# Performance work log

Measured on AMD Instinct MI355X. Metric: run time of the kernel, lower is better.

The kernel has to match this reference:

```python
import jax, jax.numpy as jnp
import numpy as np

NUM_HEADS = 12

def setup_inputs() -> dict:
    key = jax.random.key(0)
    k1, k2, k3 = jax.random.split(key, 3)
    B, T, C = 1, 4096, 768
    x = jax.random.normal(k1, (B, T, C), dtype=jnp.float32)
    w_qkv = jax.random.normal(k2, (3 * C, C), dtype=jnp.float32) * (1.0 / np.sqrt(C))
    w_proj = jax.random.normal(k3, (C, C), dtype=jnp.float32) * (1.0 / np.sqrt(C))
    attn_mask = jnp.tril(jnp.ones((T, T), dtype=bool))  # causal block mask
    return {"x": x, "w_qkv": w_qkv, "w_proj": w_proj, "attn_mask": attn_mask}


def reference(x, w_qkv, w_proj, attn_mask):
    B, T, C = x.shape
    H = NUM_HEADS
    Dh = C // H
    # fused QKV projection (torch Linear: y = x @ W.T), then split
    qkv = jnp.einsum('btc,fc->btf', x, w_qkv)  # [B,T,3C]
    q, k, v = jnp.split(qkv, 3, axis=-1)
    # [B,T,C] -> [B,H,T,Dh]
    q = q.reshape(B, T, H, Dh).transpose(0, 2, 1, 3)
    k = k.reshape(B, T, H, Dh).transpose(0, 2, 1, 3)
    v = v.reshape(B, T, H, Dh).transpose(0, 2, 1, 3)
    # masked SDPA, default flex_attention scale = 1/sqrt(head_dim)
    scores = jnp.einsum('bhqd,bhkd->bhqk', q, k) * (1.0 / np.sqrt(Dh))
    neg = jnp.finfo(scores.dtype).min
    scores = jnp.where(attn_mask[None, None, :, :], scores, neg)
    attn = jax.nn.softmax(scores, axis=-1)
    y = jnp.einsum('bhqk,bhkd->bhqd', attn, v)
    # [B,H,T,Dh] -> [B,T,C], then output projection (dropout=0)
    y = y.transpose(0, 2, 1, 3).reshape(B, T, C)
    y = jnp.einsum('btc,fc->btf', y, w_proj)
    return y
```

## Files before the change

### kernel.cpp

```cpp
#include <hip/hip_runtime.h>

typedef unsigned short u16;
typedef unsigned int u32;
typedef __attribute__((ext_vector_type(8))) short s16x8;
typedef __attribute__((ext_vector_type(4))) float f32x4;
typedef __attribute__((ext_vector_type(4))) u16 u16x4;
typedef __attribute__((ext_vector_type(4))) u32 u32x4;

#define LOG2E 1.4426950408889634f

#if __has_builtin(__builtin_amdgcn_exp2f)
#define EXP2F __builtin_amdgcn_exp2f
#else
#define EXP2F exp2f
#endif

__device__ __forceinline__ u16 f32_to_bf16(float f) {
  union { float f; u32 u; } c; c.f = f;
  return (u16)((c.u + 0x7fffu + ((c.u >> 16) & 1u)) >> 16);
}

__device__ __forceinline__ u32 pack_bf16(float lo, float hi) {
  return (u32)f32_to_bf16(lo) | ((u32)f32_to_bf16(hi) << 16);
}

__device__ __forceinline__ void async16(const void* g, void* l) {
  __builtin_amdgcn_global_load_lds(
      (__attribute__((address_space(1))) void*)g,
      (__attribute__((address_space(3))) void*)l, 16, 0, 0);
}

__global__ __launch_bounds__(256) void cast3_f32_bf16(const float* __restrict__ a,
                                                      const float* __restrict__ b,
                                                      const float* __restrict__ c,
                                                      u16* __restrict__ out,
                                                      int n1, int n2, int n3) {
  int i = (blockIdx.x * 256 + threadIdx.x) * 4;
  const float* src;
  int off = i;
  if (i < n1) {
    src = a;
  } else if (i < n1 + n2) {
    src = b; off = i - n1;
  } else if (i < n1 + n2 + n3) {
    src = c; off = i - n1 - n2;
  } else {
    return;
  }
  f32x4 v = *(const f32x4*)(src + off);
  u16x4 o;
  o[0] = f32_to_bf16(v[0]);
  o[1] = f32_to_bf16(v[1]);
  o[2] = f32_to_bf16(v[2]);
  o[3] = f32_to_bf16(v[3]);
  *(u16x4*)(out + i) = o;
}

__device__ __forceinline__ int vt_perm_inv(int k) {
  return (k & 35) | ((k & 16) >> 2) | ((k & 12) << 1);
}

__global__ __launch_bounds__(256) void qkv_gemm(const u16* __restrict__ A,
                                                const u16* __restrict__ B,
                                                u16* __restrict__ qk,
                                                u16* __restrict__ vt) {
  constexpr int K = 768;
  constexpr int BK = 32;
  constexpr int NT = K / BK;
  __shared__ alignas(16) u16 As[2][128 * BK];
  __shared__ alignas(16) u16 Bs[2][128 * BK];
  const int tid = threadIdx.x;
  const int lane = tid & 63;
  const int wid = tid >> 6;
  const int brow = blockIdx.x * 128;
  const int bcol = blockIdx.y * 128;
  const int wr = wid >> 1, wc = wid & 1;
  const int l15 = lane & 15, l4 = lane >> 4;
  f32x4 acc[4][4] = {};
  const int c0 = tid, c1 = tid + 256;
  const int r0 = c0 >> 2, s0 = c0 & 3;
  const int r1 = c1 >> 2, s1 = c1 & 3;

#define G1_STAGE(kt, b)                                                        \
  {                                                                            \
    async16(A + (size_t)(brow + r0) * K + (kt) * BK + s0 * 8, &As[b][c0 * 8]); \
    async16(A + (size_t)(brow + r1) * K + (kt) * BK + s1 * 8, &As[b][c1 * 8]); \
    async16(B + (size_t)(bcol + r0) * K + (kt) * BK + s0 * 8, &Bs[b][c0 * 8]); \
    async16(B + (size_t)(bcol + r1) * K + (kt) * BK + s1 * 8, &Bs[b][c1 * 8]); \
  }

  G1_STAGE(0, 0);
  __syncthreads();
  int cur = 0;
  for (int kt = 0; kt < NT; ++kt) {
    if (kt + 1 < NT) G1_STAGE(kt + 1, cur ^ 1);
    s16x8 af[4], bf[4];
#pragma unroll
    for (int m = 0; m < 4; ++m)
      af[m] = *(const s16x8*)&As[cur][(wr * 64 + m * 16 + l15) * BK + l4 * 8];
#pragma unroll
    for (int n = 0; n < 4; ++n)
      bf[n] = *(const s16x8*)&Bs[cur][(wc * 64 + n * 16 + l15) * BK + l4 * 8];
#pragma unroll
    for (int m = 0; m < 4; ++m)
#pragma unroll
      for (int n = 0; n < 4; ++n)
        acc[m][n] = __builtin_amdgcn_mfma_f32_16x16x32_bf16(af[m], bf[n], acc[m][n], 0, 0, 0);
    __syncthreads();
    cur ^= 1;
  }
#undef G1_STAGE

  const int row0 = brow + wr * 64 + l4 * 4;
  const int col0 = bcol + wc * 64 + l15;
  if (bcol >= 1536) {
#pragma unroll
    for (int m = 0; m < 4; ++m) {
      int t0 = row0 + m * 16;
      int s = (t0 & ~63) + vt_perm_inv(t0 & 63);
#pragma unroll
      for (int n = 0; n < 4; ++n) {
        int vcol = col0 + n * 16 - 1536;
        u16x4 pk;
#pragma unroll
        for (int r = 0; r < 4; ++r) pk[r] = f32_to_bf16(acc[m][n][r]);
        *(u16x4*)&vt[(size_t)vcol * 4096 + s] = pk;
      }
    }
  } else {
#pragma unroll
    for (int m = 0; m < 4; ++m)
#pragma unroll
      for (int n = 0; n < 4; ++n)
#pragma unroll
        for (int r = 0; r < 4; ++r)
          qk[(size_t)(row0 + m * 16 + r) * 1536 + (col0 + n * 16)] =
              f32_to_bf16(acc[m][n][r]);
  }
}

__global__ __launch_bounds__(256) void proj_gemm(const u16* __restrict__ A,
                                                 const u16* __restrict__ B,
                                                 float* __restrict__ C) {
  constexpr int K = 768;
  constexpr int N = 768;
  constexpr int BK = 32;
  constexpr int NT = K / BK;
  __shared__ alignas(16) u16 As[2][128 * BK];
  __shared__ alignas(16) u16 Bs[2][128 * BK];
  const int tid = threadIdx.x;
  const int lane = tid & 63;
  const int wid = tid >> 6;
  const int brow = blockIdx.x * 128;
  const int bcol = blockIdx.y * 128;
  const int wr = wid >> 1, wc = wid & 1;
  const int l15 = lane & 15, l4 = lane >> 4;
  f32x4 acc[4][4] = {};
  const int c0 = tid, c1 = tid + 256;
  const int r0 = c0 >> 2, s0 = c0 & 3;
  const int r1 = c1 >> 2, s1 = c1 & 3;

#define G2_STAGE(kt, b)                                                        \
  {                                                                            \
    async16(A + (size_t)(brow + r0) * K + (kt) * BK + s0 * 8, &As[b][c0 * 8]); \
    async16(A + (size_t)(brow + r1) * K + (kt) * BK + s1 * 8, &As[b][c1 * 8]); \
    async16(B + (size_t)(bcol + r0) * K + (kt) * BK + s0 * 8, &Bs[b][c0 * 8]); \
    async16(B + (size_t)(bcol + r1) * K + (kt) * BK + s1 * 8, &Bs[b][c1 * 8]); \
  }

  G2_STAGE(0, 0);
  __syncthreads();
  int cur = 0;
  for (int kt = 0; kt < NT; ++kt) {
    if (kt + 1 < NT) G2_STAGE(kt + 1, cur ^ 1);
    s16x8 af[4], bf[4];
#pragma unroll
    for (int m = 0; m < 4; ++m)
      af[m] = *(const s16x8*)&As[cur][(wr * 64 + m * 16 + l15) * BK + l4 * 8];
#pragma unroll
    for (int n = 0; n < 4; ++n)
      bf[n] = *(const s16x8*)&Bs[cur][(wc * 64 + n * 16 + l15) * BK + l4 * 8];
#pragma unroll
    for (int m = 0; m < 4; ++m)
#pragma unroll
      for (int n = 0; n < 4; ++n)
        acc[m][n] = __builtin_amdgcn_mfma_f32_16x16x32_bf16(af[m], bf[n], acc[m][n], 0, 0, 0);
    __syncthreads();
    cur ^= 1;
  }
#undef G2_STAGE

  const int row0 = brow + wr * 64 + l4 * 4;
  const int col0 = bcol + wc * 64 + l15;
#pragma unroll
  for (int m = 0; m < 4; ++m)
#pragma unroll
    for (int n = 0; n < 4; ++n)
#pragma unroll
      for (int r = 0; r < 4; ++r)
        C[(size_t)(row0 + m * 16 + r) * N + (col0 + n * 16)] = acc[m][n][r];
}

template <int C>
__global__ __launch_bounds__(256) void attn_kernel(const u16* __restrict__ qk,
                                                   const u16* __restrict__ vt,
                                                   u16* __restrict__ y,
                                                   float* __restrict__ po,
                                                   float* __restrict__ pl) {
  constexpr int MAXCH = 64 / C;
  constexpr int CPH = C * (MAXCH) * (MAXCH + 1) / 2;
  __shared__ alignas(16) u16 Ks[2][64 * 64];
  __shared__ alignas(16) u16 Vs[2][64 * 64];
  const int tid = threadIdx.x;
  const int lane = tid & 63;
  const int wid = tid >> 6;
  const int l15 = lane & 15, l4 = lane >> 4;

  int bx = blockIdx.x;
  int h = bx / CPH;
  int c = CPH - 1 - (bx % CPH);
  int g = 0;
  while (C * (g + 1) * (g + 2) / 2 <= c) ++g;
  int r_ = c - C * g * (g + 1) / 2;
  int qb = g * C + r_ / (g + 1);
  int ch = r_ % (g + 1);
  const int nch = qb / C + 1;

  const int qg = qb * 64 + wid * 16 + l15;
  const float sc = 0.125f * LOG2E;
  const float M_FIX = 16.0f;

  s16x8 bq[2];
#pragma unroll
  for (int ks = 0; ks < 2; ++ks)
    bq[ks] = *(const s16x8*)&qk[(size_t)qg * 1536 + h * 64 + ks * 32 + l4 * 8];

  f32x4 o[4] = {};
  f32x4 lacc = {};

  const u16* Kb = qk + 768 + h * 64;
  const u16* Vb = vt + (size_t)(h * 64) * 4096;

  const int sc0 = tid, sc1 = tid + 256;
  const int sr0 = sc0 >> 3, sp0 = sc0 & 7;
  const int sr1 = sc1 >> 3, sp1 = sc1 & 7;

#define STAGE_KV(t, b)                                                                        \
  {                                                                                           \
    async16(Kb + (size_t)((t) * 64 + sr0) * 1536 + ((sp0 ^ (sr0 & 7)) * 8), &Ks[b][sc0 * 8]); \
    async16(Kb + (size_t)((t) * 64 + sr1) * 1536 + ((sp1 ^ (sr1 & 7)) * 8), &Ks[b][sc1 * 8]); \
    async16(Vb + (size_t)sr0 * 4096 + (t) * 64 + ((sp0 ^ (sr0 & 7)) * 8), &Vs[b][sc0 * 8]);   \
    async16(Vb + (size_t)sr1 * 4096 + (t) * 64 + ((sp1 ^ (sr1 & 7)) * 8), &Vs[b][sc1 * 8]);   \
  }

  const int t0 = ch * C;
  const int t1 = (t0 + C < qb + 1) ? t0 + C : qb + 1;
  STAGE_KV(t0, 0);
  __syncthreads();
  int cur = 0;
  for (int kt = t0; kt < t1; ++kt) {
    if (kt + 1 < t1) STAGE_KV(kt + 1, cur ^ 1);

    f32x4 s4[4];
#pragma unroll
    for (int kf = 0; kf < 4; ++kf) {
      int r = kf * 16 + l15;
      s16x8 k0 = *(const s16x8*)&Ks[cur][r * 64 + ((l4 ^ (r & 7)) * 8)];
      s16x8 k1 = *(const s16x8*)&Ks[cur][r * 64 + (((l4 + 4) ^ (r & 7)) * 8)];
      f32x4 a = {};
      a = __builtin_amdgcn_mfma_f32_16x16x32_bf16(k0, bq[0], a, 0, 0, 0);
      a = __builtin_amdgcn_mfma_f32_16x16x32_bf16(k1, bq[1], a, 0, 0, 0);
      s4[kf] = a;
    }
    if (kt == qb) {
#pragma unroll
      for (int kf = 0; kf < 4; ++kf)
#pragma unroll
        for (int r = 0; r < 4; ++r)
          if (kt * 64 + kf * 16 + l4 * 4 + r > qg) s4[kf][r] = -1e30f;
    }
    u32 w[4][2];
#pragma unroll
    for (int kf = 0; kf < 4; ++kf) {
      f32x4 p;
#pragma unroll
      for (int r = 0; r < 4; ++r)
        p[r] = EXP2F(fmaf(s4[kf][r], sc, -M_FIX));
      lacc += p;
      w[kf][0] = pack_bf16(p[0], p[1]);
      w[kf][1] = pack_bf16(p[2], p[3]);
    }
#pragma unroll
    for (int ks2 = 0; ks2 < 2; ++ks2) {
      u32x4 bu;
      bu[0] = w[2 * ks2][0];
      bu[1] = w[2 * ks2][1];
      bu[2] = w[2 * ks2 + 1][0];
      bu[3] = w[2 * ks2 + 1][1];
      s16x8 bp = __builtin_bit_cast(s16x8, bu);
#pragma unroll
      for (int df = 0; df < 4; ++df) {
        int d = df * 16 + l15;
        int e = ks2 * 4 + l4;
        s16x8 av = *(const s16x8*)&Vs[cur][d * 64 + ((e ^ (d & 7)) * 8)];
        o[df] = __builtin_amdgcn_mfma_f32_16x16x32_bf16(av, bp, o[df], 0, 0, 0);
      }
    }
    __syncthreads();
    cur ^= 1;
  }
#undef STAGE_KV

  float lsum = lacc[0] + lacc[1] + lacc[2] + lacc[3];
  lsum += __shfl_xor(lsum, 16);
  lsum += __shfl_xor(lsum, 32);

  if (nch == 1) {
    float inv = 1.0f / lsum;
#pragma unroll
    for (int df = 0; df < 4; ++df) {
      u16x4 pk;
#pragma unroll
      for (int r = 0; r < 4; ++r) pk[r] = f32_to_bf16(o[df][r] * inv);
      *(u16x4*)&y[(size_t)qg * 768 + h * 64 + df * 16 + l4 * 4] = pk;
    }
  } else {
    const size_t slot = (size_t)(h * 64 + qb) * MAXCH + ch;
    float* ob = po + slot * 4096 + (size_t)(wid * 16 + l15) * 64;
#pragma unroll
    for (int df = 0; df < 4; ++df)
      *(f32x4*)(ob + df * 16 + l4 * 4) = o[df];
    if (lane < 16) pl[slot * 64 + wid * 16 + l15] = lsum;
  }
}

template <int C>
__global__ __launch_bounds__(256) void attn_combine(const float* __restrict__ po,
                                                    const float* __restrict__ pl,
                                                    u16* __restrict__ y) {
  constexpr int MAXCH = 64 / C;
  const int h = blockIdx.x;
  const int qb = C + blockIdx.y;
  const int nch = qb / C + 1;
  const int tid = threadIdx.x;
  const int q = tid >> 2;
  const int d0 = (tid & 3) * 16;

  f32x4 acc[4] = {};
  float lt = 0.f;
  for (int s = 0; s < nch; ++s) {
    const size_t slot = (size_t)(h * 64 + qb) * MAXCH + s;
    lt += pl[slot * 64 + q];
    const float* ob = po + slot * 4096 + (size_t)q * 64 + d0;
#pragma unroll
    for (int j = 0; j < 4; ++j) acc[j] += *(const f32x4*)(ob + j * 4);
  }
  float inv = 1.0f / lt;
  u16* yp = &y[(size_t)(qb * 64 + q) * 768 + h * 64 + d0];
#pragma unroll
  for (int j = 0; j < 4; ++j) {
    u16x4 pk;
#pragma unroll
    for (int r = 0; r < 4; ++r) pk[r] = f32_to_bf16(acc[j][r] * inv);
    *(u16x4*)(yp + j * 4) = pk;
  }
}

extern "C" void kernel_launch(void* const* d_in, const int* in_sizes, int n_in,
                              void* d_out, int out_size, void* d_ws, size_t ws_size,
                              hipStream_t stream) {
  const float* x = (const float*)d_in[0];
  const float* w_qkv = (const float*)d_in[1];
  const float* w_proj = (const float*)d_in[2];
  float* out = (float*)d_out;

  u16* ws = (u16*)d_ws;
  u16* xb = ws;
  u16* wqkvb = xb + 4096 * 768;
  u16* wprojb = wqkvb + 2304 * 768;
  u16* qkb = wprojb + 768 * 768;
  u16* vtb = qkb + (size_t)4096 * 1536;
  u16* yb = vtb + (size_t)768 * 4096;
  const size_t base_u16 = (size_t)4096 * 768 + 2304 * 768 + 768 * 768 +
                          (size_t)4096 * 1536 + (size_t)768 * 4096 + (size_t)4096 * 768;
  float* pf = (float*)(ws + base_u16);
  const size_t base_b = base_u16 * 2;

  constexpr int N1 = 4096 * 768, N2 = 2304 * 768, N3 = 768 * 768;
  cast3_f32_bf16<<<(N1 + N2 + N3) / 4 / 256, 256, 0, stream>>>(
      x, w_qkv, w_proj, xb, N1, N2, N3);

  qkv_gemm<<<dim3(32, 18), 256, 0, stream>>>(xb, wqkvb, qkb, vtb);

  const size_t need16 = base_b + (size_t)(12 * 64 * 4) * (4096 + 64) * 4;
  const size_t need32 = base_b + (size_t)(12 * 64 * 2) * (4096 + 64) * 4;
  if (ws_size >= need16) {
    constexpr int C = 16, MAXCH = 64 / C, CPH = C * MAXCH * (MAXCH + 1) / 2;
    float* po = pf;
    float* pl = po + (size_t)12 * 64 * MAXCH * 4096;
    attn_kernel<C><<<12 * CPH, 256, 0, stream>>>(qkb, vtb, yb, po, pl);
    attn_combine<C><<<dim3(12, 64 - C), 256, 0, stream>>>(po, pl, yb);
  } else if (ws_size >= need32) {
    constexpr int C = 32, MAXCH = 64 / C, CPH = C * MAXCH * (MAXCH + 1) / 2;
    float* po = pf;
    float* pl = po + (size_t)12 * 64 * MAXCH * 4096;
    attn_kernel<C><<<12 * CPH, 256, 0, stream>>>(qkb, vtb, yb, po, pl);
    attn_combine<C><<<dim3(12, 64 - C), 256, 0, stream>>>(po, pl, yb);
  } else {
    constexpr int C = 64, MAXCH = 1, CPH = 64;
    attn_kernel<C><<<12 * CPH, 256, 0, stream>>>(qkb, vtb, yb, nullptr, nullptr);
  }

  proj_gemm<<<dim3(32, 6), 256, 0, stream>>>(yb, wprojb, out);
}
```

Measured before the change: 134.8 us.

## Double query tile per attention block and fold softmax scale into Q projection

```diff
diff --git a/kernel.cpp b/kernel.cpp
--- a/kernel.cpp
+++ b/kernel.cpp
@@ -20,8 +20,10 @@
   return (u16)((c.u + 0x7fffu + ((c.u >> 16) & 1u)) >> 16);
 }
 
-__device__ __forceinline__ u32 pack_bf16(float lo, float hi) {
-  return (u32)f32_to_bf16(lo) | ((u32)f32_to_bf16(hi) << 16);
+__device__ __forceinline__ u32 cvtpk(float lo, float hi) {
+  u32 r;
+  asm("v_cvt_pk_bf16_f32 %0, %1, %2" : "=v"(r) : "v"(lo), "v"(hi));
+  return r;
 }
 
 __device__ __forceinline__ void async16(const void* g, void* l) {
@@ -128,6 +130,7 @@
       }
     }
   } else {
+    const float qs = (bcol < 768) ? 0.125f * LOG2E : 1.0f;
 #pragma unroll
     for (int m = 0; m < 4; ++m)
 #pragma unroll
@@ -135,7 +138,7 @@
 #pragma unroll
         for (int r = 0; r < 4; ++r)
           qk[(size_t)(row0 + m * 16 + r) * 1536 + (col0 + n * 16)] =
-              f32_to_bf16(acc[m][n][r]);
+              f32_to_bf16(acc[m][n][r] * qs);
   }
 }
 
@@ -201,14 +204,20 @@
         C[(size_t)(row0 + m * 16 + r) * N + (col0 + n * 16)] = acc[m][n][r];
 }
 
+constexpr int cph_for(int C) {
+  int s = 0;
+  for (int qb = 0; qb < 32; ++qb) s += (2 * qb + 2 + C - 1) / C;
+  return s;
+}
+
 template <int C>
 __global__ __launch_bounds__(256) void attn_kernel(const u16* __restrict__ qk,
                                                    const u16* __restrict__ vt,
                                                    u16* __restrict__ y,
                                                    float* __restrict__ po,
                                                    float* __restrict__ pl) {
-  constexpr int MAXCH = 64 / C;
-  constexpr int CPH = C * (MAXCH) * (MAXCH + 1) / 2;
+  constexpr int MAXCH = (64 + C - 1) / C;
+  constexpr int CPH = cph_for(C);
   __shared__ alignas(16) u16 Ks[2][64 * 64];
   __shared__ alignas(16) u16 Vs[2][64 * 64];
   const int tid = threadIdx.x;
@@ -216,27 +225,30 @@
   const int wid = tid >> 6;
   const int l15 = lane & 15, l4 = lane >> 4;
 
-  int bx = blockIdx.x;
-  int h = bx / CPH;
-  int c = CPH - 1 - (bx % CPH);
-  int g = 0;
-  while (C * (g + 1) * (g + 2) / 2 <= c) ++g;
-  int r_ = c - C * g * (g + 1) / 2;
-  int qb = g * C + r_ / (g + 1);
-  int ch = r_ % (g + 1);
-  const int nch = qb / C + 1;
-
-  const int qg = qb * 64 + wid * 16 + l15;
-  const float sc = 0.125f * LOG2E;
-  const float M_FIX = 16.0f;
-
-  s16x8 bq[2];
-#pragma unroll
-  for (int ks = 0; ks < 2; ++ks)
-    bq[ks] = *(const s16x8*)&qk[(size_t)qg * 1536 + h * 64 + ks * 32 + l4 * 8];
-
-  f32x4 o[4] = {};
-  f32x4 lacc = {};
+  const int h = blockIdx.x % 12;
+  int c = CPH - 1 - (int)(blockIdx.x / 12);
+  int qb = 0, ch = c;
+  for (;;) {
+    int n = (2 * qb + 2 + C - 1) / C;
+    if (ch < n) break;
+    ch -= n;
+    ++qb;
+  }
+  const int NTt = 2 * qb + 2;
+  const int nch = (NTt + C - 1) / C;
+
+  const int qw0 = qb * 128 + wid * 32;
+
+  s16x8 bq[2][2];
+#pragma unroll
+  for (int qf = 0; qf < 2; ++qf)
+#pragma unroll
+    for (int ks = 0; ks < 2; ++ks)
+      bq[qf][ks] = *(const s16x8*)&qk[(size_t)(qw0 + qf * 16 + l15) * 1536 +
+                                      h * 64 + ks * 32 + l4 * 8];
+
+  f32x4 o[2][4] = {};
+  f32x4 lacc[2] = {};
 
   const u16* Kb = qk + 768 + h * 64;
   const u16* Vb = vt + (size_t)(h * 64) * 4096;
@@ -254,56 +266,70 @@
   }
 
   const int t0 = ch * C;
-  const int t1 = (t0 + C < qb + 1) ? t0 + C : qb + 1;
+  const int t1 = (t0 + C < NTt) ? t0 + C : NTt;
   STAGE_KV(t0, 0);
   __syncthreads();
   int cur = 0;
   for (int kt = t0; kt < t1; ++kt) {
     if (kt + 1 < t1) STAGE_KV(kt + 1, cur ^ 1);
 
-    f32x4 s4[4];
+    f32x4 s4[2][4];
 #pragma unroll
     for (int kf = 0; kf < 4; ++kf) {
       int r = kf * 16 + l15;
       s16x8 k0 = *(const s16x8*)&Ks[cur][r * 64 + ((l4 ^ (r & 7)) * 8)];
       s16x8 k1 = *(const s16x8*)&Ks[cur][r * 64 + (((l4 + 4) ^ (r & 7)) * 8)];
-      f32x4 a = {};
-      a = __builtin_amdgcn_mfma_f32_16x16x32_bf16(k0, bq[0], a, 0, 0, 0);
-      a = __builtin_amdgcn_mfma_f32_16x16x32_bf16(k1, bq[1], a, 0, 0, 0);
-      s4[kf] = a;
-    }
-    if (kt == qb) {
-#pragma unroll
-      for (int kf = 0; kf < 4; ++kf)
-#pragma unroll
-        for (int r = 0; r < 4; ++r)
-          if (kt * 64 + kf * 16 + l4 * 4 + r > qg) s4[kf][r] = -1e30f;
-    }
-    u32 w[4][2];
-#pragma unroll
-    for (int kf = 0; kf < 4; ++kf) {
-      f32x4 p;
-#pragma unroll
-      for (int r = 0; r < 4; ++r)
-        p[r] = EXP2F(fmaf(s4[kf][r], sc, -M_FIX));
-      lacc += p;
-      w[kf][0] = pack_bf16(p[0], p[1]);
-      w[kf][1] = pack_bf16(p[2], p[3]);
-    }
+#pragma unroll
+      for (int qf = 0; qf < 2; ++qf) {
+        f32x4 a = {};
+        a = __builtin_amdgcn_mfma_f32_16x16x32_bf16(k0, bq[qf][0], a, 0, 0, 0);
+        a = __builtin_amdgcn_mfma_f32_16x16x32_bf16(k1, bq[qf][1], a, 0, 0, 0);
+        s4[qf][kf] = a;
+      }
+    }
+    if (kt >= 2 * qb) {
+#pragma unroll
+      for (int qf = 0; qf < 2; ++qf) {
+        int qg = qw0 + qf * 16 + l15;
+#pragma unroll
+        for (int kf = 0; kf < 4; ++kf)
+#pragma unroll
+          for (int r = 0; r < 4; ++r)
+            if (kt * 64 + kf * 16 + l4 * 4 + r > qg) s4[qf][kf][r] = -1e30f;
+      }
+    }
+    u32 w[2][4][2];
+#pragma unroll
+    for (int qf = 0; qf < 2; ++qf)
+#pragma unroll
+      for (int kf = 0; kf < 4; ++kf) {
+        f32x4 p;
+#pragma unroll
+        for (int r = 0; r < 4; ++r) p[r] = EXP2F(s4[qf][kf][r]);
+        lacc[qf] += p;
+        w[qf][kf][0] = cvtpk(p[0], p[1]);
+        w[qf][kf][1] = cvtpk(p[2], p[3]);
+      }
 #pragma unroll
     for (int ks2 = 0; ks2 < 2; ++ks2) {
-      u32x4 bu;
-      bu[0] = w[2 * ks2][0];
-      bu[1] = w[2 * ks2][1];
-      bu[2] = w[2 * ks2 + 1][0];
-      bu[3] = w[2 * ks2 + 1][1];
-      s16x8 bp = __builtin_bit_cast(s16x8, bu);
+      s16x8 bp[2];
+#pragma unroll
+      for (int qf = 0; qf < 2; ++qf) {
+        u32x4 bu;
+        bu[0] = w[qf][2 * ks2][0];
+        bu[1] = w[qf][2 * ks2][1];
+        bu[2] = w[qf][2 * ks2 + 1][0];
+        bu[3] = w[qf][2 * ks2 + 1][1];
+        bp[qf] = __builtin_bit_cast(s16x8, bu);
+      }
 #pragma unroll
       for (int df = 0; df < 4; ++df) {
         int d = df * 16 + l15;
         int e = ks2 * 4 + l4;
         s16x8 av = *(const s16x8*)&Vs[cur][d * 64 + ((e ^ (d & 7)) * 8)];
-        o[df] = __builtin_amdgcn_mfma_f32_16x16x32_bf16(av, bp, o[df], 0, 0, 0);
+#pragma unroll
+        for (int qf = 0; qf < 2; ++qf)
+          o[qf][df] = __builtin_amdgcn_mfma_f32_16x16x32_bf16(av, bp[qf], o[qf][df], 0, 0, 0);
       }
     }
     __syncthreads();
@@ -311,26 +337,37 @@
   }
 #undef STAGE_KV
 
-  float lsum = lacc[0] + lacc[1] + lacc[2] + lacc[3];
-  lsum += __shfl_xor(lsum, 16);
-  lsum += __shfl_xor(lsum, 32);
+  float lsum[2];
+#pragma unroll
+  for (int qf = 0; qf < 2; ++qf) {
+    float s = lacc[qf][0] + lacc[qf][1] + lacc[qf][2] + lacc[qf][3];
+    s += __shfl_xor(s, 16);
+    s += __shfl_xor(s, 32);
+    lsum[qf] = s;
+  }
 
   if (nch == 1) {
-    float inv = 1.0f / lsum;
-#pragma unroll
-    for (int df = 0; df < 4; ++df) {
-      u16x4 pk;
-#pragma unroll
-      for (int r = 0; r < 4; ++r) pk[r] = f32_to_bf16(o[df][r] * inv);
-      *(u16x4*)&y[(size_t)qg * 768 + h * 64 + df * 16 + l4 * 4] = pk;
+#pragma unroll
+    for (int qf = 0; qf < 2; ++qf) {
+      float inv = 1.0f / lsum[qf];
+#pragma unroll
+      for (int df = 0; df < 4; ++df) {
+        u16x4 pk;
+#pragma unroll
+        for (int r = 0; r < 4; ++r) pk[r] = f32_to_bf16(o[qf][df][r] * inv);
+        *(u16x4*)&y[(size_t)(qw0 + qf * 16 + l15) * 768 + h * 64 + df * 16 + l4 * 4] = pk;
+      }
     }
   } else {
-    const size_t slot = (size_t)(h * 64 + qb) * MAXCH + ch;
-    float* ob = po + slot * 4096 + (size_t)(wid * 16 + l15) * 64;
-#pragma unroll
-    for (int df = 0; df < 4; ++df)
-      *(f32x4*)(ob + df * 16 + l4 * 4) = o[df];
-    if (lane < 16) pl[slot * 64 + wid * 16 + l15] = lsum;
+    const size_t slot = (size_t)(h * 32 + qb) * MAXCH + ch;
+#pragma unroll
+    for (int qf = 0; qf < 2; ++qf) {
+      float* ob = po + slot * 8192 + (size_t)(wid * 32 + qf * 16 + l15) * 64;
+#pragma unroll
+      for (int df = 0; df < 4; ++df)
+        *(f32x4*)(ob + df * 16 + l4 * 4) = o[qf][df];
+      if (lane < 16) pl[slot * 128 + wid * 32 + qf * 16 + l15] = lsum[qf];
+    }
   }
 }
 
@@ -338,27 +375,27 @@
 __global__ __launch_bounds__(256) void attn_combine(const float* __restrict__ po,
                                                     const float* __restrict__ pl,
                                                     u16* __restrict__ y) {
-  constexpr int MAXCH = 64 / C;
+  constexpr int MAXCH = (64 + C - 1) / C;
   const int h = blockIdx.x;
-  const int qb = C + blockIdx.y;
-  const int nch = qb / C + 1;
+  const int qb = C / 2 + blockIdx.y;
+  const int nch = (2 * qb + 2 + C - 1) / C;
   const int tid = threadIdx.x;
-  const int q = tid >> 2;
-  const int d0 = (tid & 3) * 16;
-
-  f32x4 acc[4] = {};
+  const int q = tid >> 1;
+  const int d0 = (tid & 1) * 32;
+
+  f32x4 acc[8] = {};
   float lt = 0.f;
   for (int s = 0; s < nch; ++s) {
-    const size_t slot = (size_t)(h * 64 + qb) * MAXCH + s;
-    lt += pl[slot * 64 + q];
-    const float* ob = po + slot * 4096 + (size_t)q * 64 + d0;
-#pragma unroll
-    for (int j = 0; j < 4; ++j) acc[j] += *(const f32x4*)(ob + j * 4);
+    const size_t slot = (size_t)(h * 32 + qb) * MAXCH + s;
+    lt += pl[slot * 128 + q];
+    const float* ob = po + slot * 8192 + (size_t)q * 64 + d0;
+#pragma unroll
+    for (int j = 0; j < 8; ++j) acc[j] += *(const f32x4*)(ob + j * 4);
   }
   float inv = 1.0f / lt;
-  u16* yp = &y[(size_t)(qb * 64 + q) * 768 + h * 64 + d0];
-#pragma unroll
-  for (int j = 0; j < 4; ++j) {
+  u16* yp = &y[(size_t)(qb * 128 + q) * 768 + h * 64 + d0];
+#pragma unroll
+  for (int j = 0; j < 8; ++j) {
     u16x4 pk;
 #pragma unroll
     for (int r = 0; r < 4; ++r) pk[r] = f32_to_bf16(acc[j][r] * inv);
@@ -392,23 +429,23 @@
 
   qkv_gemm<<<dim3(32, 18), 256, 0, stream>>>(xb, wqkvb, qkb, vtb);
 
-  const size_t need16 = base_b + (size_t)(12 * 64 * 4) * (4096 + 64) * 4;
-  const size_t need32 = base_b + (size_t)(12 * 64 * 2) * (4096 + 64) * 4;
+  const size_t need16 = base_b + (size_t)(12 * 32 * 4) * (8192 + 128) * 4;
+  const size_t need32 = base_b + (size_t)(12 * 32 * 2) * (8192 + 128) * 4;
   if (ws_size >= need16) {
-    constexpr int C = 16, MAXCH = 64 / C, CPH = C * MAXCH * (MAXCH + 1) / 2;
+    constexpr int C = 16, MAXCH = 4;
     float* po = pf;
-    float* pl = po + (size_t)12 * 64 * MAXCH * 4096;
-    attn_kernel<C><<<12 * CPH, 256, 0, stream>>>(qkb, vtb, yb, po, pl);
-    attn_combine<C><<<dim3(12, 64 - C), 256, 0, stream>>>(po, pl, yb);
+    float* pl = po + (size_t)12 * 32 * MAXCH * 8192;
+    attn_kernel<C><<<12 * cph_for(C), 256, 0, stream>>>(qkb, vtb, yb, po, pl);
+    attn_combine<C><<<dim3(12, 32 - C / 2), 256, 0, stream>>>(po, pl, yb);
   } else if (ws_size >= need32) {
-    constexpr int C = 32, MAXCH = 64 / C, CPH = C * MAXCH * (MAXCH + 1) / 2;
+    constexpr int C = 32, MAXCH = 2;
     float* po = pf;
-    float* pl = po + (size_t)12 * 64 * MAXCH * 4096;
-    attn_kernel<C><<<12 * CPH, 256, 0, stream>>>(qkb, vtb, yb, po, pl);
-    attn_combine<C><<<dim3(12, 64 - C), 256, 0, stream>>>(po, pl, yb);
+    float* pl = po + (size_t)12 * 32 * MAXCH * 8192;
+    attn_kernel<C><<<12 * cph_for(C), 256, 0, stream>>>(qkb, vtb, yb, po, pl);
+    attn_combine<C><<<dim3(12, 32 - C / 2), 256, 0, stream>>>(po, pl, yb);
   } else {
-    constexpr int C = 64, MAXCH = 1, CPH = 64;
-    attn_kernel<C><<<12 * CPH, 256, 0, stream>>>(qkb, vtb, yb, nullptr, nullptr);
+    constexpr int C = 64;
+    attn_kernel<C><<<12 * cph_for(C), 256, 0, stream>>>(qkb, vtb, yb, nullptr, nullptr);
   }
 
   proj_gemm<<<dim3(32, 6), 256, 0, stream>>>(yb, wprojb, out);
```

After: 119.5 us. 1.13x faster.
